# Performance work log

Measured on AMD Instinct MI355X. Metric: run time of the kernel, lower is better.

Reference implementation:

```python
import jax, jax.numpy as jnp
import numpy as np

K = 3
DILATION = 1
DG = 1  # deformable groups


def _deform_conv2d(x, offsets, mask, weight, bias, k=K, dilation=DILATION, dg=DG):
    # x: [B, C, H, W]; offsets: [B, dg*2*k*k, H, W]; mask: [B, dg*k*k, H, W]
    # weight: [O, C, k, k]; bias: [O]
    B, C, H, W = x.shape
    O = weight.shape[0]
    Cg = C // dg
    kk = k * k
    pad = (k // 2) * dilation

    # base sampling grid per kernel tap (stride=1)
    ky, kx = jnp.meshgrid(jnp.arange(k), jnp.arange(k), indexing='ij')
    ky = ky.reshape(kk)
    kx = kx.reshape(kk)
    base_y = (jnp.arange(H)[None, :, None] - pad + ky[:, None, None] * dilation)  # [kk,H,1]
    base_x = (jnp.arange(W)[None, None, :] - pad + kx[:, None, None] * dilation)  # [kk,1,W]

    off = offsets.reshape(B, dg, kk, 2, H, W)
    py = base_y[None, None].astype(x.dtype) + off[:, :, :, 0]  # [B,dg,kk,H,W]
    px = base_x[None, None].astype(x.dtype) + off[:, :, :, 1]  # [B,dg,kk,H,W]

    y0 = jnp.floor(py)
    x0 = jnp.floor(px)
    wy1 = py - y0  # frac weights
    wx1 = px - x0
    wy0 = 1.0 - wy1
    wx0 = 1.0 - wx1

    img = x.reshape(B, dg, Cg, H * W)

    def gather(yi, xi):
        # yi, xi: float integer-valued coords [B,dg,kk,H,W]; zero outside bounds
        valid = (yi >= 0) & (yi <= H - 1) & (xi >= 0) & (xi <= W - 1)
        yc = jnp.clip(yi, 0, H - 1).astype(jnp.int32)
        xc = jnp.clip(xi, 0, W - 1).astype(jnp.int32)
        idx = (yc * W + xc).reshape(B, dg, 1, kk * H * W)
        vals = jnp.take_along_axis(img, idx, axis=3).reshape(B, dg, Cg, kk, H, W)
        return vals * valid.reshape(B, dg, 1, kk, H, W).astype(x.dtype)

    def w5(a):  # lift [B,dg,kk,H,W] -> [B,dg,1,kk,H,W]
        return a.reshape(B, dg, 1, kk, H, W)

    sampled = (gather(y0, x0) * w5(wy0 * wx0)
               + gather(y0, x0 + 1) * w5(wy0 * wx1)
               + gather(y0 + 1, x0) * w5(wy1 * wx0)
               + gather(y0 + 1, x0 + 1) * w5(wy1 * wx1))  # [B,dg,Cg,kk,H,W]

    sampled = sampled * mask.reshape(B, dg, 1, kk, H, W)
    sampled = sampled.reshape(B, C, kk, H, W)

    out = jnp.einsum('bckhw,ock->bohw', sampled, weight.reshape(O, C, kk))
    return out + bias[None, :, None, None]


def setup_inputs() -> dict:
    key = jax.random.key(0)
    k1, k2, k3, k4, k5 = jax.random.split(key, 5)
    B, C, O, H, W = 8, 128, 128, 64, 64
    x = jax.random.normal(k1, (B, C, H, W), dtype=jnp.float32)
    offsets = jax.random.normal(k2, (B, DG * 2 * K * K, H, W), dtype=jnp.float32)
    mask = jax.random.uniform(k3, (B, DG * K * K, H, W), dtype=jnp.float32)
    fan_in = C * K * K
    weight = jax.random.normal(k4, (O, C, K, K), dtype=jnp.float32) / np.sqrt(fan_in)
    bias = jax.random.normal(k5, (O,), dtype=jnp.float32) * 0.01
    return {"x": x, "offsets": offsets, "mask": mask, "weight": weight, "bias": bias}


def reference(x, offsets, mask, weight, bias):
    return _deform_conv2d(x, offsets, mask, weight, bias)
```

## Files before the change

kernel.cpp:

```cpp
#include <hip/hip_runtime.h>
#include <math.h>

constexpr int Bn = 8, Cn = 128, On = 128, Hn = 64, Wn = 64;
constexpr int KK = 9, PAD = 1;
constexpr int BDIM = 512;
constexpr int PXB  = 64;
constexpr int CG = 16, NG = Cn / CG;
constexpr int KG = 160, KTOT = NG * KG;
constexpr int BANDH = 11;
constexpr int RST  = 68;
constexpr int XSTP = 756;
constexpr int AST  = 84;
constexpr int ME   = KK * PXB;
constexpr int PB_DW  = 8 * XSTP;
constexpr int ASH_DW = PXB * AST;
constexpr int SM_DW  = PB_DW + 2 * ASH_DW;
constexpr int BUNITS = BANDH * 128;

typedef __attribute__((ext_vector_type(2))) _Float16 h2;
typedef __attribute__((ext_vector_type(8))) __fp16   f16x8;
typedef __attribute__((ext_vector_type(4))) float f32x4;
typedef unsigned short u16;
typedef unsigned int u32;

union UH  { u32 u; h2 h; };
union U4H { uint4 u; f16x8 h; };

__device__ __forceinline__ u32 pkh(float a, float b) {
    union { decltype(__builtin_amdgcn_cvt_pkrtz(0.f, 0.f)) p; u32 u; } t;
    t.p = __builtin_amdgcn_cvt_pkrtz(a, b);
    return t.u;
}
__device__ __forceinline__ h2 bch(u32 w) { UH t; t.u = w; return t.h; }
__device__ __forceinline__ u16 f2h(float f) {
    union { _Float16 h; u16 u; } v; v.h = (_Float16)f; return v.u;
}

__global__ void wprep_kernel(const float* __restrict__ w, u16* __restrict__ wh) {
    __shared__ u32 tmpw[KTOT / 2];
    u16* tmp = (u16*)tmpw;
    const int tid = threadIdx.x, o = blockIdx.x;
    if (tid < 64)
        tmpw[(tid >> 3) * 80 + 72 + (tid & 7)] = 0;
    for (int k = tid; k < Cn * KK; k += 256) {
        const int c = k / 9, t = k - 9 * c;
        tmp[(c >> 4) * KG + t * 16 + (c & 15)] = f2h(w[o * (Cn * KK) + k]);
    }
    __syncthreads();
    u32* dst = (u32*)(wh + (size_t)o * KTOT);
    for (int e = tid; e < KTOT / 2; e += 256) dst[e] = tmpw[e];
}

__device__ __forceinline__ void do_sample(const u32* __restrict__ pband,
                                          u32* __restrict__ ashW,
                                          const float* __restrict__ xg,
                                          const uint4 wp, const int2 q,
                                          const int2 ix, const int e)
{
    const int t = e >> 6, px = e & 63;
    u32 avp[8];
    if (!__any((q.x | q.y) < 0)) {
        const u32* p0 = pband + ix.x;
        const u32* p1 = pband + ix.y;
        const h2 w0 = bch(wp.x), w1 = bch(wp.y), w2 = bch(wp.z), w3 = bch(wp.w);
        #pragma unroll
        for (int c2 = 0; c2 < 8; ++c2) {
            const h2 vt0 = bch(p0[c2 * XSTP]), vt1 = bch(p0[c2 * XSTP + 1]);
            const h2 vb0 = bch(p1[c2 * XSTP]), vb1 = bch(p1[c2 * XSTP + 1]);
            const h2 r = w0 * vt0 + w1 * vt1 + w2 * vb0 + w3 * vb1;
            UH o; o.h = r; avp[c2] = o.u;
        }
    } else {
        const float fw0 = (float)bch(wp.x)[0], fw1 = (float)bch(wp.y)[0];
        const float fw2 = (float)bch(wp.z)[0], fw3 = (float)bch(wp.w)[0];
        const int qx = q.x < 0 ? ~q.x : q.x;
        const int qy = q.y < 0 ? ~q.y : q.y;
        const int yrx = qx >> 8, yry = qy >> 8;
        const int xx = (qx & 255) - 1, xy = (qy & 255) - 1;
        const int ax0 = max(xx, 0), ax1 = min(xx + 1, Wn - 1);
        const int ay0 = max(xy, 0), ay1 = min(xy + 1, Wn - 1);
        #pragma unroll
        for (int c2 = 0; c2 < 8; ++c2) {
            float v2[2];
            #pragma unroll
            for (int sb = 0; sb < 2; ++sb) {
                const float* gc = xg + ((2 * c2 + sb) << 12);
                const float t0 = gc[yrx * Wn + ax0], t1 = gc[yrx * Wn + ax1];
                const float b0 = gc[yry * Wn + ay0], b1 = gc[yry * Wn + ay1];
                v2[sb] = fmaf(fw0, t0, fmaf(fw1, t1, fmaf(fw2, b0, fw3 * b1)));
            }
            avp[c2] = pkh(v2[0], v2[1]);
        }
    }
    u32* d = ashW + px * AST + t * 8;
    *(uint4*)&d[0] = make_uint4(avp[0], avp[1], avp[2], avp[3]);
    *(uint4*)&d[4] = make_uint4(avp[4], avp[5], avp[6], avp[7]);
}

__global__ __launch_bounds__(BDIM, 4)
void dcn_mfma_kernel(const float* __restrict__ x,
                     const float* __restrict__ offs,
                     const float* __restrict__ mask,
                     const u16*   __restrict__ wh,
                     const float* __restrict__ bias,
                     float* __restrict__ out)
{
    __shared__ __align__(16) u32 smem[SM_DW];
    u32* const pband = smem;

    const int tid = threadIdx.x;
    const int b   = blockIdx.x & 7;
    const int h   = blockIdx.x >> 3;
    const int r0  = min(max(h - 5, 0), Hn - BANDH);

    const int s_px4 = tid & 15, s_pair = (tid >> 4) & 7;

    float4 bnda[3], bndb[3];
#define BLOAD(GCH) { \
        _Pragma("unroll") \
        for (int it = 0; it < 3; ++it) { \
            const int u = tid + it * BDIM; \
            if (u < BUNITS) { \
                const int row = u >> 7; \
                const float* bp = x + (((size_t)(b * Cn + (GCH) * CG + 2 * s_pair)) << 12) \
                                  + (r0 + row) * Wn + (s_px4 << 2); \
                bnda[it] = *(const float4*)bp; \
                bndb[it] = *(const float4*)(bp + 4096); \
            } \
        } }
#define BWRITE() { \
        _Pragma("unroll") \
        for (int it = 0; it < 3; ++it) { \
            const int u = tid + it * BDIM; \
            if (u < BUNITS) { \
                const int row = u >> 7; \
                u32* d = &pband[s_pair * XSTP + row * RST + 8 + (s_px4 << 2)]; \
                *(uint4*)d = make_uint4( \
                    pkh(bnda[it].x, bndb[it].x), pkh(bnda[it].y, bndb[it].y), \
                    pkh(bnda[it].z, bndb[it].z), pkh(bnda[it].w, bndb[it].w)); \
            } \
        } }

    BLOAD(0);

    uint4 mwp[2]; int2 mq[2]; int2 mi[2];
    #pragma unroll
    for (int it = 0; it < 2; ++it) {
        mwp[it] = make_uint4(0, 0, 0, 0);
        mq[it] = make_int2(r0 << 8, r0 << 8);
        mi[it] = make_int2(7, 7);
        const int e = tid + it * BDIM;
        if (e < ME) {
            const int t = e >> 6, px = e & 63;
            const int ty = t / 3, tx = t - ty * 3;
            const float oy = offs[((b * 18 + 2 * t    ) * Hn + h) * Wn + px];
            const float ox = offs[((b * 18 + 2 * t + 1) * Hn + h) * Wn + px];
            const float m  = mask[((b * KK + t) * Hn + h) * Wn + px];
            const float py = (float)(h - PAD + ty) + oy;
            const float qx = (float)(px - PAD + tx) + ox;
            const float fy = floorf(py), fx = floorf(qx);
            const float wy1 = py - fy, wx1 = qx - fx;
            const float wy0 = 1.f - wy1, wx0 = 1.f - wx1;
            const int y0 = (int)fy, x0 = (int)fx;
            const bool cx0 = (x0 >= 0) && (x0 < Wn);
            const bool cx1 = (x0 >= -1) && (x0 < Wn - 1);
            const float wr[2] = { wy0, wy1 };
            float wout[4]; int qout[2], iout[2];
            #pragma unroll
            for (int j = 0; j < 2; ++j) {
                const int yr = y0 + j;
                const bool rv = (yr >= 0) && (yr < Hn);
                wout[2 * j]     = (rv && cx0) ? wr[j] * wx0 * m : 0.f;
                wout[2 * j + 1] = (rv && cx1) ? wr[j] * wx1 * m : 0.f;
                int qv;
                if (!rv || (!cx0 && !cx1)) qv = r0 << 8;
                else                       qv = (yr << 8) | (x0 + 1);
                const bool inband = (qv >> 8) >= r0 && (qv >> 8) < r0 + BANDH;
                qout[j] = inband ? qv : ~qv;
                iout[j] = ((qv >> 8) - r0) * RST + (qv & 255) + 7;
            }
            mwp[it] = make_uint4(pkh(wout[0], wout[0]), pkh(wout[1], wout[1]),
                                 pkh(wout[2], wout[2]), pkh(wout[3], wout[3]));
            mq[it] = make_int2(qout[0], qout[1]);
            mi[it] = make_int2(iout[0], iout[1]);
        }
    }

    if (tid < 416) {
        const int pair = tid / 52, j = tid - pair * 52;
        const int off = (j < 8) ? j : RST * ((j - 8) >> 2) + 72 + ((j - 8) & 3);
        pband[pair * XSTP + off] = 0;
    }
    #pragma unroll
    for (int it = 0; it < 2; ++it) {
        const int u = tid + it * BDIM;
        smem[PB_DW + (u >> 9) * ASH_DW + ((u & 511) >> 3) * AST + 72 + (u & 7)] = 0;
    }

    BWRITE();
    BLOAD(1);
    __syncthreads();

    const int wv = tid >> 6, ln = tid & 63, quad = ln >> 4, l16 = ln & 15;
    const int mrow = wv >> 1, ncol = wv & 1;
    const u16* wrow0 = wh + (size_t)(mrow * 32 + l16) * KTOT;
    const int npx0 = ncol * 32 + l16, npx1 = npx0 + 16;

    {
        const float* xg = x + (((size_t)(b * Cn)) << 12);
        do_sample(pband, smem + PB_DW, xg, mwp[0], mq[0], mi[0], tid);
        if (tid < 64)
            do_sample(pband, smem + PB_DW, xg, mwp[1], mq[1], mi[1], BDIM + tid);
    }
    __syncthreads();

    f32x4 acc[2][2];
    #pragma unroll
    for (int mt = 0; mt < 2; ++mt)
        #pragma unroll
        for (int nt = 0; nt < 2; ++nt) acc[mt][nt] = (f32x4){0.f, 0.f, 0.f, 0.f};

    f16x8 pa[5][2];
#define APRE(GG) { const int kgp = (GG) * KG + quad * 8; \
        _Pragma("unroll") \
        for (int s = 0; s < 5; ++s) { \
            pa[s][0] = *(const f16x8*)(wrow0 + kgp + s * 32); \
            pa[s][1] = *(const f16x8*)(wrow0 + 16 * KTOT + kgp + s * 32); \
        } }
    APRE(0);

#define MSTEP(S) { \
        const int kd = (S) * 16 + quad * 4; \
        U4H b0, b1; \
        b0.u = *(const uint4*)&ad[npx0 * AST + kd]; \
        b1.u = *(const uint4*)&ad[npx1 * AST + kd]; \
        acc[0][0] = __builtin_amdgcn_mfma_f32_16x16x32_f16(pa[S][0], b0.h, acc[0][0], 0, 0, 0); \
        acc[0][1] = __builtin_amdgcn_mfma_f32_16x16x32_f16(pa[S][0], b1.h, acc[0][1], 0, 0, 0); \
        acc[1][0] = __builtin_amdgcn_mfma_f32_16x16x32_f16(pa[S][1], b0.h, acc[1][0], 0, 0, 0); \
        acc[1][1] = __builtin_amdgcn_mfma_f32_16x16x32_f16(pa[S][1], b1.h, acc[1][1], 0, 0, 0); }

    for (int g = 0; g < NG; ++g) {
        const u32* ad = smem + PB_DW + (g & 1) * ASH_DW;
        u32* ashN     = smem + PB_DW + ((g + 1) & 1) * ASH_DW;
        if (g + 1 < NG) BWRITE();
        MSTEP(0);
        MSTEP(1);
        __syncthreads();
        if (g + 2 < NG) BLOAD(g + 2);
        if (g + 1 < NG) {
            const float* xg = x + (((size_t)(b * Cn + (g + 1) * CG)) << 12);
            do_sample(pband, ashN, xg, mwp[0], mq[0], mi[0], tid);
            if (tid < 64)
                do_sample(pband, ashN, xg, mwp[1], mq[1], mi[1], BDIM + tid);
        }
        MSTEP(2);
        MSTEP(3);
        MSTEP(4);
        if (g + 1 < NG) APRE(g + 1);
        __syncthreads();
    }

    float* tr = (float*)smem;
    #pragma unroll
    for (int mt = 0; mt < 2; ++mt)
        #pragma unroll
        for (int nt = 0; nt < 2; ++nt)
            #pragma unroll
            for (int r = 0; r < 4; ++r) {
                const int o  = mrow * 32 + mt * 16 + quad * 4 + r;
                const int px = ncol * 32 + nt * 16 + l16;
                tr[o * 68 + px] = acc[mt][nt][r] + bias[o];
            }
    __syncthreads();
    {
        const int orow = tid >> 2, f0 = tid & 3;
        #pragma unroll
        for (int it = 0; it < 4; ++it) {
            const int f = f0 + it * 4;
            const float4 v = *(const float4*)&tr[orow * 68 + (f << 2)];
            *(float4*)&out[(((size_t)b * On + orow) * Hn + h) * Wn + (f << 2)] = v;
        }
    }
#undef BLOAD
#undef BWRITE
#undef APRE
#undef MSTEP
}

constexpr int FBD = 256;
constexpr int FB_PXB = 32, FB_CCH = 4, FB_NCT = FB_CCH * KK, FB_MW = KK * FB_PXB;

#define FMA4(A, S, W)                          \
    A.x = fmaf((S).x, (W), A.x);               \
    A.y = fmaf((S).y, (W), A.y);               \
    A.z = fmaf((S).z, (W), A.z);               \
    A.w = fmaf((S).w, (W), A.w);

__global__ __launch_bounds__(FBD, 4)
void dcn_fb_kernel(const float* __restrict__ x,
                   const float* __restrict__ offs,
                   const float* __restrict__ mask,
                   const float* __restrict__ weight,
                   const float* __restrict__ bias,
                   float* __restrict__ out)
{
    __shared__ float wmeta[4 * FB_MW];
    __shared__ int   imeta[4 * FB_MW];
    __shared__ float ssh[FB_NCT * FB_PXB];
    __shared__ float wsh[FB_NCT * On];

    const int tid    = threadIdx.x;
    const int b      = blockIdx.x & 7;
    const int rem    = blockIdx.x >> 3;
    const int h      = rem >> 1;
    const int pxbase = (rem & 1) * FB_PXB;

    for (int e = tid; e < FB_MW; e += FBD) {
        const int t  = e >> 5;
        const int px = e & 31;
        const int pg = pxbase + px;
        const int ty = t / 3, tx = t - ty * 3;
        const float oy = offs[((b * 18 + 2 * t    ) * Hn + h) * Wn + pg];
        const float ox = offs[((b * 18 + 2 * t + 1) * Hn + h) * Wn + pg];
        const float m  = mask[((b * KK + t) * Hn + h) * Wn + pg];
        const float py = (float)(h - PAD + ty) + oy;
        const float qx = (float)(pg - PAD + tx) + ox;
        const float y0 = floorf(py), x0 = floorf(qx);
        const float wy1 = py - y0, wx1 = qx - x0;
        const float wy0 = 1.f - wy1, wx0 = 1.f - wx1;
        const float cw[4] = { wy0 * wx0, wy0 * wx1, wy1 * wx0, wy1 * wx1 };
        #pragma unroll
        for (int k = 0; k < 4; ++k) {
            const float yk = y0 + (float)(k >> 1);
            const float xk = x0 + (float)(k & 1);
            const bool valid = (yk >= 0.f) && (yk <= (float)(Hn - 1)) &&
                               (xk >= 0.f) && (xk <= (float)(Wn - 1));
            const int yc = (int)fminf(fmaxf(yk, 0.f), (float)(Hn - 1));
            const int xc = (int)fminf(fmaxf(xk, 0.f), (float)(Wn - 1));
            wmeta[k * FB_MW + e] = valid ? cw[k] * m : 0.f;
            imeta[k * FB_MW + e] = yc * Wn + xc;
        }
    }
    __syncthreads();

    const int px0 = (tid & 7) << 2;
    const int oo  = (tid >> 3) << 2;

    float4 acc[4];
    #pragma unroll
    for (int j = 0; j < 4; ++j) acc[j] = make_float4(0.f, 0.f, 0.f, 0.f);

    for (int cb = 0; cb < Cn / FB_CCH; ++cb) {
        #pragma unroll
        for (int it = 0; it < (FB_NCT * On) / FBD; ++it) {
            const int e = tid + it * FBD;
            const int r = e >> 7;
            const int o = e & 127;
            wsh[r * On + o] = weight[o * (Cn * KK) + cb * FB_NCT + r];
        }
        for (int e = tid; e < FB_NCT * FB_PXB; e += FBD) {
            const int px = e & 31;
            const int ct = e >> 5;
            const int c  = ct / 9;
            const int mb = (ct - c * 9) * FB_PXB + px;
            const float* xp = x + (((b * Cn) + cb * FB_CCH + c) << 12);
            float v =  wmeta[mb]              * xp[imeta[mb]];
            v = fmaf(wmeta[FB_MW     + mb], xp[imeta[FB_MW     + mb]], v);
            v = fmaf(wmeta[2 * FB_MW + mb], xp[imeta[2 * FB_MW + mb]], v);
            v = fmaf(wmeta[3 * FB_MW + mb], xp[imeta[3 * FB_MW + mb]], v);
            ssh[ct * FB_PXB + px] = v;
        }
        __syncthreads();

        #pragma unroll 6
        for (int ct = 0; ct < FB_NCT; ++ct) {
            const float4 sv = *(const float4*)&ssh[ct * FB_PXB + px0];
            const float4 wa = *(const float4*)&wsh[ct * On + oo];
            FMA4(acc[0], sv, wa.x);
            FMA4(acc[1], sv, wa.y);
            FMA4(acc[2], sv, wa.z);
            FMA4(acc[3], sv, wa.w);
        }
        __syncthreads();
    }

    #pragma unroll
    for (int j = 0; j < 4; ++j) {
        const float bv = bias[oo + j];
        float4 r = acc[j];
        r.x += bv; r.y += bv; r.z += bv; r.w += bv;
        *(float4*)&out[((b * On + oo + j) * Hn + h) * Wn + pxbase + px0] = r;
    }
}

extern "C" void kernel_launch(void* const* d_in, const int* in_sizes, int n_in,
                              void* d_out, int out_size, void* d_ws, size_t ws_size,
                              hipStream_t stream) {
    const float* x      = (const float*)d_in[0];
    const float* offs   = (const float*)d_in[1];
    const float* mask   = (const float*)d_in[2];
    const float* weight = (const float*)d_in[3];
    const float* bias   = (const float*)d_in[4];
    float* out = (float*)d_out;

    const size_t need = (size_t)On * KTOT * sizeof(u16);
    if (d_ws != nullptr && ws_size >= need) {
        u16* wh = (u16*)d_ws;
        wprep_kernel<<<dim3(On), dim3(256), 0, stream>>>(weight, wh);
        dcn_mfma_kernel<<<dim3(Bn * Hn), dim3(BDIM), 0, stream>>>(
            x, offs, mask, wh, bias, out);
    } else {
        dcn_fb_kernel<<<dim3(Bn * Hn * 2), dim3(FBD), 0, stream>>>(
            x, offs, mask, weight, bias, out);
    }
}
```

Measured before the change: 149.9 us.

## Split each row into two 32-pixel blocks with 8-channel groups and higher occupancy

Restructures the MFMA deformable-conv kernel so each block handles 32 pixels of a row instead of 64, which doubles the grid to 1024 blocks. Channel groups shrink from 16 to 8 (16 groups), and the shared-memory band and sample buffers are resized to match. Each wave now owns 16 output channels against 2 pixel tiles, the A operand is loaded from global memory inside every MFMA step instead of being prefetched, and launch bounds rise to 8 blocks per CU. The aim is more parallelism and occupancy. The cost is that every block reloads the same 11-row input band, so band traffic doubles, and there are more barriers per unit of work.

```diff
diff --git a/kernel.cpp b/kernel.cpp
--- a/kernel.cpp
+++ b/kernel.cpp
@@ -4,18 +4,21 @@
 constexpr int Bn = 8, Cn = 128, On = 128, Hn = 64, Wn = 64;
 constexpr int KK = 9, PAD = 1;
 constexpr int BDIM = 512;
-constexpr int PXB  = 64;
-constexpr int CG = 16, NG = Cn / CG;
-constexpr int KG = 160, KTOT = NG * KG;
 constexpr int BANDH = 11;
 constexpr int RST  = 68;
 constexpr int XSTP = 756;
-constexpr int AST  = 84;
-constexpr int ME   = KK * PXB;
-constexpr int PB_DW  = 8 * XSTP;
-constexpr int ASH_DW = PXB * AST;
-constexpr int SM_DW  = PB_DW + 2 * ASH_DW;
-constexpr int BUNITS = BANDH * 128;
+
+constexpr int PXB3 = 32;
+constexpr int CG3  = 8,  NG3 = 16;
+constexpr int KG3  = 96;
+constexpr int KT3  = NG3 * KG3;
+constexpr int AST3 = 52;
+constexpr int ME3  = KK * PXB3;
+constexpr int PB3_DW  = 4 * XSTP;
+constexpr int ASH3_DW = PXB3 * AST3;
+constexpr int SM3_DW  = PB3_DW + 2 * ASH3_DW;
+constexpr int BU3  = BANDH * 64;
+constexpr size_t WH3_BYTES = (size_t)On * KT3 * 2;
 
 typedef __attribute__((ext_vector_type(2))) _Float16 h2;
 typedef __attribute__((ext_vector_type(8))) __fp16   f16x8;
@@ -36,35 +39,36 @@
     union { _Float16 h; u16 u; } v; v.h = (_Float16)f; return v.u;
 }
 
-__global__ void wprep_kernel(const float* __restrict__ w, u16* __restrict__ wh) {
-    __shared__ u32 tmpw[KTOT / 2];
-    u16* tmp = (u16*)tmpw;
+__global__ void wprep3_kernel(const float* __restrict__ w, u16* __restrict__ wh3) {
+    __shared__ u16 tmp[KT3];
     const int tid = threadIdx.x, o = blockIdx.x;
-    if (tid < 64)
-        tmpw[(tid >> 3) * 80 + 72 + (tid & 7)] = 0;
+    for (int e = tid; e < 384; e += 256) {
+        const int g = e / 24, j = e - g * 24;
+        tmp[g * 96 + 72 + j] = 0;
+    }
     for (int k = tid; k < Cn * KK; k += 256) {
         const int c = k / 9, t = k - 9 * c;
-        tmp[(c >> 4) * KG + t * 16 + (c & 15)] = f2h(w[o * (Cn * KK) + k]);
-    }
-    __syncthreads();
-    u32* dst = (u32*)(wh + (size_t)o * KTOT);
-    for (int e = tid; e < KTOT / 2; e += 256) dst[e] = tmpw[e];
-}
-
-__device__ __forceinline__ void do_sample(const u32* __restrict__ pband,
-                                          u32* __restrict__ ashW,
-                                          const float* __restrict__ xg,
-                                          const uint4 wp, const int2 q,
-                                          const int2 ix, const int e)
+        tmp[(c >> 3) * 96 + t * 8 + (c & 7)] = f2h(w[o * (Cn * KK) + k]);
+    }
+    __syncthreads();
+    u32* dst = (u32*)(wh3 + (size_t)o * KT3);
+    for (int e = tid; e < KT3 / 2; e += 256) dst[e] = ((u32*)tmp)[e];
+}
+
+__device__ __forceinline__ void sample3(const u32* __restrict__ pband,
+                                        u32* __restrict__ ashW,
+                                        const float* __restrict__ xg,
+                                        const uint4 wp, const int2 q,
+                                        const int2 ix, const int tid)
 {
-    const int t = e >> 6, px = e & 63;
-    u32 avp[8];
+    const int t = tid >> 5, px = tid & 31;
+    u32 avp[4];
     if (!__any((q.x | q.y) < 0)) {
         const u32* p0 = pband + ix.x;
         const u32* p1 = pband + ix.y;
         const h2 w0 = bch(wp.x), w1 = bch(wp.y), w2 = bch(wp.z), w3 = bch(wp.w);
         #pragma unroll
-        for (int c2 = 0; c2 < 8; ++c2) {
+        for (int c2 = 0; c2 < 4; ++c2) {
             const h2 vt0 = bch(p0[c2 * XSTP]), vt1 = bch(p0[c2 * XSTP + 1]);
             const h2 vb0 = bch(p1[c2 * XSTP]), vb1 = bch(p1[c2 * XSTP + 1]);
             const h2 r = w0 * vt0 + w1 * vt1 + w2 * vb0 + w3 * vb1;
@@ -80,7 +84,7 @@
         const int ax0 = max(xx, 0), ax1 = min(xx + 1, Wn - 1);
         const int ay0 = max(xy, 0), ay1 = min(xy + 1, Wn - 1);
         #pragma unroll
-        for (int c2 = 0; c2 < 8; ++c2) {
+        for (int c2 = 0; c2 < 4; ++c2) {
             float v2[2];
             #pragma unroll
             for (int sb = 0; sb < 2; ++sb) {
@@ -92,101 +96,93 @@
             avp[c2] = pkh(v2[0], v2[1]);
         }
     }
-    u32* d = ashW + px * AST + t * 8;
-    *(uint4*)&d[0] = make_uint4(avp[0], avp[1], avp[2], avp[3]);
-    *(uint4*)&d[4] = make_uint4(avp[4], avp[5], avp[6], avp[7]);
-}
-
-__global__ __launch_bounds__(BDIM, 4)
-void dcn_mfma_kernel(const float* __restrict__ x,
-                     const float* __restrict__ offs,
-                     const float* __restrict__ mask,
-                     const u16*   __restrict__ wh,
-                     const float* __restrict__ bias,
-                     float* __restrict__ out)
+    *(uint4*)(ashW + px * AST3 + t * 4) = make_uint4(avp[0], avp[1], avp[2], avp[3]);
+}
+
+__global__ __launch_bounds__(BDIM, 8)
+void dcn_cg8_kernel(const float* __restrict__ x,
+                    const float* __restrict__ offs,
+                    const float* __restrict__ mask,
+                    const u16*   __restrict__ wh3,
+                    const float* __restrict__ bias,
+                    float* __restrict__ out)
 {
-    __shared__ __align__(16) u32 smem[SM_DW];
+    __shared__ __align__(16) u32 smem[SM3_DW];
     u32* const pband = smem;
 
-    const int tid = threadIdx.x;
-    const int b   = blockIdx.x & 7;
-    const int h   = blockIdx.x >> 3;
-    const int r0  = min(max(h - 5, 0), Hn - BANDH);
-
-    const int s_px4 = tid & 15, s_pair = (tid >> 4) & 7;
-
-    float4 bnda[3], bndb[3];
-#define BLOAD(GCH) { \
+    const int tid    = threadIdx.x;
+    const int b      = blockIdx.x & 7;
+    const int h      = (blockIdx.x >> 3) & 63;
+    const int pxbase = (blockIdx.x >> 9) * PXB3;
+    const int r0     = min(max(h - 5, 0), Hn - BANDH);
+
+    float4 bnda[2], bndb[2];
+#define BLOAD3(GCH) { \
         _Pragma("unroll") \
-        for (int it = 0; it < 3; ++it) { \
+        for (int it = 0; it < 2; ++it) { \
             const int u = tid + it * BDIM; \
-            if (u < BUNITS) { \
-                const int row = u >> 7; \
-                const float* bp = x + (((size_t)(b * Cn + (GCH) * CG + 2 * s_pair)) << 12) \
-                                  + (r0 + row) * Wn + (s_px4 << 2); \
+            if (u < BU3) { \
+                const int px4 = u & 15, pair = (u >> 4) & 3, row = u >> 6; \
+                const float* bp = x + (((size_t)(b * Cn + (GCH) * CG3 + 2 * pair)) << 12) \
+                                  + (r0 + row) * Wn + (px4 << 2); \
                 bnda[it] = *(const float4*)bp; \
                 bndb[it] = *(const float4*)(bp + 4096); \
             } \
         } }
-#define BWRITE() { \
+#define BWRITE3() { \
         _Pragma("unroll") \
-        for (int it = 0; it < 3; ++it) { \
+        for (int it = 0; it < 2; ++it) { \
             const int u = tid + it * BDIM; \
-            if (u < BUNITS) { \
-                const int row = u >> 7; \
-                u32* d = &pband[s_pair * XSTP + row * RST + 8 + (s_px4 << 2)]; \
+            if (u < BU3) { \
+                const int px4 = u & 15, pair = (u >> 4) & 3, row = u >> 6; \
+                u32* d = &pband[pair * XSTP + row * RST + 8 + (px4 << 2)]; \
                 *(uint4*)d = make_uint4( \
                     pkh(bnda[it].x, bndb[it].x), pkh(bnda[it].y, bndb[it].y), \
                     pkh(bnda[it].z, bndb[it].z), pkh(bnda[it].w, bndb[it].w)); \
             } \
         } }
 
-    BLOAD(0);
-
-    uint4 mwp[2]; int2 mq[2]; int2 mi[2];
-    #pragma unroll
-    for (int it = 0; it < 2; ++it) {
-        mwp[it] = make_uint4(0, 0, 0, 0);
-        mq[it] = make_int2(r0 << 8, r0 << 8);
-        mi[it] = make_int2(7, 7);
-        const int e = tid + it * BDIM;
-        if (e < ME) {
-            const int t = e >> 6, px = e & 63;
-            const int ty = t / 3, tx = t - ty * 3;
-            const float oy = offs[((b * 18 + 2 * t    ) * Hn + h) * Wn + px];
-            const float ox = offs[((b * 18 + 2 * t + 1) * Hn + h) * Wn + px];
-            const float m  = mask[((b * KK + t) * Hn + h) * Wn + px];
-            const float py = (float)(h - PAD + ty) + oy;
-            const float qx = (float)(px - PAD + tx) + ox;
-            const float fy = floorf(py), fx = floorf(qx);
-            const float wy1 = py - fy, wx1 = qx - fx;
-            const float wy0 = 1.f - wy1, wx0 = 1.f - wx1;
-            const int y0 = (int)fy, x0 = (int)fx;
-            const bool cx0 = (x0 >= 0) && (x0 < Wn);
-            const bool cx1 = (x0 >= -1) && (x0 < Wn - 1);
-            const float wr[2] = { wy0, wy1 };
-            float wout[4]; int qout[2], iout[2];
-            #pragma unroll
-            for (int j = 0; j < 2; ++j) {
-                const int yr = y0 + j;
-                const bool rv = (yr >= 0) && (yr < Hn);
-                wout[2 * j]     = (rv && cx0) ? wr[j] * wx0 * m : 0.f;
-                wout[2 * j + 1] = (rv && cx1) ? wr[j] * wx1 * m : 0.f;
-                int qv;
-                if (!rv || (!cx0 && !cx1)) qv = r0 << 8;
-                else                       qv = (yr << 8) | (x0 + 1);
-                const bool inband = (qv >> 8) >= r0 && (qv >> 8) < r0 + BANDH;
-                qout[j] = inband ? qv : ~qv;
-                iout[j] = ((qv >> 8) - r0) * RST + (qv & 255) + 7;
-            }
-            mwp[it] = make_uint4(pkh(wout[0], wout[0]), pkh(wout[1], wout[1]),
-                                 pkh(wout[2], wout[2]), pkh(wout[3], wout[3]));
-            mq[it] = make_int2(qout[0], qout[1]);
-            mi[it] = make_int2(iout[0], iout[1]);
-        }
-    }
-
-    if (tid < 416) {
+    BLOAD3(0);
+
+    uint4 mwp = make_uint4(0, 0, 0, 0);
+    int2 mq = make_int2(r0 << 8, r0 << 8);
+    int2 mi = make_int2(7, 7);
+    if (tid < ME3) {
+        const int t = tid >> 5, px = tid & 31, pg = pxbase + px;
+        const int ty = t / 3, tx = t - ty * 3;
+        const float oy = offs[((b * 18 + 2 * t    ) * Hn + h) * Wn + pg];
+        const float ox = offs[((b * 18 + 2 * t + 1) * Hn + h) * Wn + pg];
+        const float m  = mask[((b * KK + t) * Hn + h) * Wn + pg];
+        const float py = (float)(h - PAD + ty) + oy;
+        const float qx = (float)(pg - PAD + tx) + ox;
+        const float fy = floorf(py), fx = floorf(qx);
+        const float wy1 = py - fy, wx1 = qx - fx;
+        const float wy0 = 1.f - wy1, wx0 = 1.f - wx1;
+        const int y0 = (int)fy, x0 = (int)fx;
+        const bool cx0 = (x0 >= 0) && (x0 < Wn);
+        const bool cx1 = (x0 >= -1) && (x0 < Wn - 1);
+        const float wr[2] = { wy0, wy1 };
+        float wout[4]; int qout[2], iout[2];
+        #pragma unroll
+        for (int j = 0; j < 2; ++j) {
+            const int yr = y0 + j;
+            const bool rv = (yr >= 0) && (yr < Hn);
+            wout[2 * j]     = (rv && cx0) ? wr[j] * wx0 * m : 0.f;
+            wout[2 * j + 1] = (rv && cx1) ? wr[j] * wx1 * m : 0.f;
+            int qv;
+            if (!rv || (!cx0 && !cx1)) qv = r0 << 8;
+            else                       qv = (yr << 8) | (x0 + 1);
+            const bool inband = (qv >> 8) >= r0 && (qv >> 8) < r0 + BANDH;
+            qout[j] = inband ? qv : ~qv;
+            iout[j] = ((qv >> 8) - r0) * RST + (qv & 255) + 7;
+        }
+        mwp = make_uint4(pkh(wout[0], wout[0]), pkh(wout[1], wout[1]),
+                         pkh(wout[2], wout[2]), pkh(wout[3], wout[3]));
+        mq = make_int2(qout[0], qout[1]);
+        mi = make_int2(iout[0], iout[1]);
+    }
+
+    if (tid < 208) {
         const int pair = tid / 52, j = tid - pair * 52;
         const int off = (j < 8) ? j : RST * ((j - 8) >> 2) + 72 + ((j - 8) & 3);
         pband[pair * XSTP + off] = 0;
@@ -194,97 +190,74 @@
     #pragma unroll
     for (int it = 0; it < 2; ++it) {
         const int u = tid + it * BDIM;
-        smem[PB_DW + (u >> 9) * ASH_DW + ((u & 511) >> 3) * AST + 72 + (u & 7)] = 0;
-    }
-
-    BWRITE();
-    BLOAD(1);
+        if (u < 768) {
+            const int buf = u / 384, rem = u - buf * 384;
+            const int px = rem / 12, j = rem - px * 12;
+            smem[PB3_DW + buf * ASH3_DW + px * AST3 + 36 + j] = 0;
+        }
+    }
+
+    BWRITE3();
+    BLOAD3(1);
     __syncthreads();
 
     const int wv = tid >> 6, ln = tid & 63, quad = ln >> 4, l16 = ln & 15;
-    const int mrow = wv >> 1, ncol = wv & 1;
-    const u16* wrow0 = wh + (size_t)(mrow * 32 + l16) * KTOT;
-    const int npx0 = ncol * 32 + l16, npx1 = npx0 + 16;
-
-    {
-        const float* xg = x + (((size_t)(b * Cn)) << 12);
-        do_sample(pband, smem + PB_DW, xg, mwp[0], mq[0], mi[0], tid);
-        if (tid < 64)
-            do_sample(pband, smem + PB_DW, xg, mwp[1], mq[1], mi[1], BDIM + tid);
-    }
-    __syncthreads();
-
-    f32x4 acc[2][2];
-    #pragma unroll
-    for (int mt = 0; mt < 2; ++mt)
-        #pragma unroll
-        for (int nt = 0; nt < 2; ++nt) acc[mt][nt] = (f32x4){0.f, 0.f, 0.f, 0.f};
-
-    f16x8 pa[5][2];
-#define APRE(GG) { const int kgp = (GG) * KG + quad * 8; \
-        _Pragma("unroll") \
-        for (int s = 0; s < 5; ++s) { \
-            pa[s][0] = *(const f16x8*)(wrow0 + kgp + s * 32); \
-            pa[s][1] = *(const f16x8*)(wrow0 + 16 * KTOT + kgp + s * 32); \
-        } }
-    APRE(0);
-
-#define MSTEP(S) { \
-        const int kd = (S) * 16 + quad * 4; \
+    const u16* wrow = wh3 + (size_t)(wv * 16 + l16) * KT3;
+
+    if (tid < ME3)
+        sample3(pband, smem + PB3_DW, x + (((size_t)(b * Cn)) << 12),
+                mwp, mq, mi, tid);
+    __syncthreads();
+
+    f32x4 acc[2];
+    acc[0] = (f32x4){0.f, 0.f, 0.f, 0.f};
+    acc[1] = (f32x4){0.f, 0.f, 0.f, 0.f};
+
+#define MSTEP3(S) { \
+        const f16x8 a = *(const f16x8*)(wrow + g * KG3 + (S) * 32 + quad * 8); \
         U4H b0, b1; \
-        b0.u = *(const uint4*)&ad[npx0 * AST + kd]; \
-        b1.u = *(const uint4*)&ad[npx1 * AST + kd]; \
-        acc[0][0] = __builtin_amdgcn_mfma_f32_16x16x32_f16(pa[S][0], b0.h, acc[0][0], 0, 0, 0); \
-        acc[0][1] = __builtin_amdgcn_mfma_f32_16x16x32_f16(pa[S][0], b1.h, acc[0][1], 0, 0, 0); \
-        acc[1][0] = __builtin_amdgcn_mfma_f32_16x16x32_f16(pa[S][1], b0.h, acc[1][0], 0, 0, 0); \
-        acc[1][1] = __builtin_amdgcn_mfma_f32_16x16x32_f16(pa[S][1], b1.h, acc[1][1], 0, 0, 0); }
-
-    for (int g = 0; g < NG; ++g) {
-        const u32* ad = smem + PB_DW + (g & 1) * ASH_DW;
-        u32* ashN     = smem + PB_DW + ((g + 1) & 1) * ASH_DW;
-        if (g + 1 < NG) BWRITE();
-        MSTEP(0);
-        MSTEP(1);
+        b0.u = *(const uint4*)&ad[l16 * AST3 + (S) * 16 + quad * 4]; \
+        b1.u = *(const uint4*)&ad[(16 + l16) * AST3 + (S) * 16 + quad * 4]; \
+        acc[0] = __builtin_amdgcn_mfma_f32_16x16x32_f16(a, b0.h, acc[0], 0, 0, 0); \
+        acc[1] = __builtin_amdgcn_mfma_f32_16x16x32_f16(a, b1.h, acc[1], 0, 0, 0); }
+
+    for (int g = 0; g < NG3; ++g) {
+        const u32* ad = smem + PB3_DW + (g & 1) * ASH3_DW;
+        u32* ashN     = smem + PB3_DW + ((g + 1) & 1) * ASH3_DW;
+        if (g + 1 < NG3) BWRITE3();
+        MSTEP3(0);
         __syncthreads();
-        if (g + 2 < NG) BLOAD(g + 2);
-        if (g + 1 < NG) {
-            const float* xg = x + (((size_t)(b * Cn + (g + 1) * CG)) << 12);
-            do_sample(pband, ashN, xg, mwp[0], mq[0], mi[0], tid);
-            if (tid < 64)
-                do_sample(pband, ashN, xg, mwp[1], mq[1], mi[1], BDIM + tid);
-        }
-        MSTEP(2);
-        MSTEP(3);
-        MSTEP(4);
-        if (g + 1 < NG) APRE(g + 1);
+        if (g + 2 < NG3) BLOAD3(g + 2);
+        if (g + 1 < NG3 && tid < ME3)
+            sample3(pband, ashN,
+                    x + (((size_t)(b * Cn + (g + 1) * CG3)) << 12),
+                    mwp, mq, mi, tid);
+        MSTEP3(1);
+        MSTEP3(2);
         __syncthreads();
     }
 
     float* tr = (float*)smem;
     #pragma unroll
-    for (int mt = 0; mt < 2; ++mt)
-        #pragma unroll
-        for (int nt = 0; nt < 2; ++nt)
-            #pragma unroll
-            for (int r = 0; r < 4; ++r) {
-                const int o  = mrow * 32 + mt * 16 + quad * 4 + r;
-                const int px = ncol * 32 + nt * 16 + l16;
-                tr[o * 68 + px] = acc[mt][nt][r] + bias[o];
-            }
+    for (int nt = 0; nt < 2; ++nt)
+        #pragma unroll
+        for (int r = 0; r < 4; ++r) {
+            const int o = wv * 16 + quad * 4 + r;
+            tr[o * 36 + nt * 16 + l16] = acc[nt][r] + bias[o];
+        }
     __syncthreads();
     {
-        const int orow = tid >> 2, f0 = tid & 3;
-        #pragma unroll
-        for (int it = 0; it < 4; ++it) {
-            const int f = f0 + it * 4;
-            const float4 v = *(const float4*)&tr[orow * 68 + (f << 2)];
-            *(float4*)&out[(((size_t)b * On + orow) * Hn + h) * Wn + (f << 2)] = v;
-        }
-    }
-#undef BLOAD
-#undef BWRITE
-#undef APRE
-#undef MSTEP
+        const int f = tid & 7;
+        #pragma unroll
+        for (int it = 0; it < 2; ++it) {
+            const int o = it * 64 + (tid >> 3);
+            *(float4*)&out[(((size_t)b * On + o) << 12) + h * Wn + pxbase + (f << 2)]
+                = *(const float4*)&tr[o * 36 + (f << 2)];
+        }
+    }
+#undef BLOAD3
+#undef BWRITE3
+#undef MSTEP3
 }
 
 constexpr int FBD = 256;
@@ -403,12 +376,11 @@
     const float* bias   = (const float*)d_in[4];
     float* out = (float*)d_out;
 
-    const size_t need = (size_t)On * KTOT * sizeof(u16);
-    if (d_ws != nullptr && ws_size >= need) {
-        u16* wh = (u16*)d_ws;
-        wprep_kernel<<<dim3(On), dim3(256), 0, stream>>>(weight, wh);
-        dcn_mfma_kernel<<<dim3(Bn * Hn), dim3(BDIM), 0, stream>>>(
-            x, offs, mask, wh, bias, out);
+    if (d_ws != nullptr && ws_size >= WH3_BYTES) {
+        u16* wh3 = (u16*)d_ws;
+        wprep3_kernel<<<dim3(On), dim3(256), 0, stream>>>(weight, wh3);
+        dcn_cg8_kernel<<<dim3(2 * Bn * Hn), dim3(BDIM), 0, stream>>>(
+            x, offs, mask, wh3, bias, out);
     } else {
         dcn_fb_kernel<<<dim3(Bn * Hn * 2), dim3(FBD), 0, stream>>>(
             x, offs, mask, weight, bias, out);
```

Result: slower. 170.5 us (+13.7%).

## Single-buffer sampled tile and load weight fragments per MFMA step

Applied to the files above, without the earlier changes.

Replaces the double-buffered sampled-activation LDS tile with a single buffer. Each group is now sampled, synchronised, then consumed, instead of sampling the next group while the current one is multiplied. The register-held weight prefetch array (pa[5][2]) is dropped and weight fragments are loaded from global memory inside each MFMA step. This cuts LDS use and register pressure, which may raise occupancy, but it gives up the overlap between sampling and matrix math and puts global-load latency directly in front of the MFMAs.

```diff
diff --git a/kernel.cpp b/kernel.cpp
--- a/kernel.cpp
+++ b/kernel.cpp
@@ -14,8 +14,9 @@
 constexpr int ME   = KK * PXB;
 constexpr int PB_DW  = 8 * XSTP;
 constexpr int ASH_DW = PXB * AST;
-constexpr int SM_DW  = PB_DW + 2 * ASH_DW;
+constexpr int SM_DW  = PB_DW + ASH_DW;
 constexpr int BUNITS = BANDH * 128;
+constexpr size_t WH_BYTES = (size_t)On * KTOT * 2;
 
 typedef __attribute__((ext_vector_type(2))) _Float16 h2;
 typedef __attribute__((ext_vector_type(8))) __fp16   f16x8;
@@ -107,6 +108,7 @@
 {
     __shared__ __align__(16) u32 smem[SM_DW];
     u32* const pband = smem;
+    u32* const ash   = smem + PB_DW;
 
     const int tid = threadIdx.x;
     const int b   = blockIdx.x & 7;
@@ -191,11 +193,7 @@
         const int off = (j < 8) ? j : RST * ((j - 8) >> 2) + 72 + ((j - 8) & 3);
         pband[pair * XSTP + off] = 0;
     }
-    #pragma unroll
-    for (int it = 0; it < 2; ++it) {
-        const int u = tid + it * BDIM;
-        smem[PB_DW + (u >> 9) * ASH_DW + ((u & 511) >> 3) * AST + 72 + (u & 7)] = 0;
-    }
+    ash[(tid >> 3) * AST + 72 + (tid & 7)] = 0;
 
     BWRITE();
     BLOAD(1);
@@ -206,57 +204,40 @@
     const u16* wrow0 = wh + (size_t)(mrow * 32 + l16) * KTOT;
     const int npx0 = ncol * 32 + l16, npx1 = npx0 + 16;
 
-    {
-        const float* xg = x + (((size_t)(b * Cn)) << 12);
-        do_sample(pband, smem + PB_DW, xg, mwp[0], mq[0], mi[0], tid);
-        if (tid < 64)
-            do_sample(pband, smem + PB_DW, xg, mwp[1], mq[1], mi[1], BDIM + tid);
-    }
-    __syncthreads();
-
     f32x4 acc[2][2];
     #pragma unroll
     for (int mt = 0; mt < 2; ++mt)
         #pragma unroll
         for (int nt = 0; nt < 2; ++nt) acc[mt][nt] = (f32x4){0.f, 0.f, 0.f, 0.f};
 
-    f16x8 pa[5][2];
-#define APRE(GG) { const int kgp = (GG) * KG + quad * 8; \
-        _Pragma("unroll") \
-        for (int s = 0; s < 5; ++s) { \
-            pa[s][0] = *(const f16x8*)(wrow0 + kgp + s * 32); \
-            pa[s][1] = *(const f16x8*)(wrow0 + 16 * KTOT + kgp + s * 32); \
-        } }
-    APRE(0);
-
 #define MSTEP(S) { \
+        const int kg = g * KG + (S) * 32 + quad * 8; \
+        const f16x8 a0 = *(const f16x8*)(wrow0 + kg); \
+        const f16x8 a1 = *(const f16x8*)(wrow0 + 16 * KTOT + kg); \
         const int kd = (S) * 16 + quad * 4; \
         U4H b0, b1; \
-        b0.u = *(const uint4*)&ad[npx0 * AST + kd]; \
-        b1.u = *(const uint4*)&ad[npx1 * AST + kd]; \
-        acc[0][0] = __builtin_amdgcn_mfma_f32_16x16x32_f16(pa[S][0], b0.h, acc[0][0], 0, 0, 0); \
-        acc[0][1] = __builtin_amdgcn_mfma_f32_16x16x32_f16(pa[S][0], b1.h, acc[0][1], 0, 0, 0); \
-        acc[1][0] = __builtin_amdgcn_mfma_f32_16x16x32_f16(pa[S][1], b0.h, acc[1][0], 0, 0, 0); \
-        acc[1][1] = __builtin_amdgcn_mfma_f32_16x16x32_f16(pa[S][1], b1.h, acc[1][1], 0, 0, 0); }
+        b0.u = *(const uint4*)&ash[npx0 * AST + kd]; \
+        b1.u = *(const uint4*)&ash[npx1 * AST + kd]; \
+        acc[0][0] = __builtin_amdgcn_mfma_f32_16x16x32_f16(a0, b0.h, acc[0][0], 0, 0, 0); \
+        acc[0][1] = __builtin_amdgcn_mfma_f32_16x16x32_f16(a0, b1.h, acc[0][1], 0, 0, 0); \
+        acc[1][0] = __builtin_amdgcn_mfma_f32_16x16x32_f16(a1, b0.h, acc[1][0], 0, 0, 0); \
+        acc[1][1] = __builtin_amdgcn_mfma_f32_16x16x32_f16(a1, b1.h, acc[1][1], 0, 0, 0); }
 
     for (int g = 0; g < NG; ++g) {
-        const u32* ad = smem + PB_DW + (g & 1) * ASH_DW;
-        u32* ashN     = smem + PB_DW + ((g + 1) & 1) * ASH_DW;
+        {
+            const float* xg = x + (((size_t)(b * Cn + g * CG)) << 12);
+            do_sample(pband, ash, xg, mwp[0], mq[0], mi[0], tid);
+            if (tid < 64)
+                do_sample(pband, ash, xg, mwp[1], mq[1], mi[1], BDIM + tid);
+        }
+        __syncthreads();
         if (g + 1 < NG) BWRITE();
+        if (g + 2 < NG) BLOAD(g + 2);
         MSTEP(0);
         MSTEP(1);
-        __syncthreads();
-        if (g + 2 < NG) BLOAD(g + 2);
-        if (g + 1 < NG) {
-            const float* xg = x + (((size_t)(b * Cn + (g + 1) * CG)) << 12);
-            do_sample(pband, ashN, xg, mwp[0], mq[0], mi[0], tid);
-            if (tid < 64)
-                do_sample(pband, ashN, xg, mwp[1], mq[1], mi[1], BDIM + tid);
-        }
         MSTEP(2);
         MSTEP(3);
         MSTEP(4);
-        if (g + 1 < NG) APRE(g + 1);
         __syncthreads();
     }
 
@@ -283,7 +264,6 @@
     }
 #undef BLOAD
 #undef BWRITE
-#undef APRE
 #undef MSTEP
 }
 
@@ -403,8 +383,7 @@
     const float* bias   = (const float*)d_in[4];
     float* out = (float*)d_out;
 
-    const size_t need = (size_t)On * KTOT * sizeof(u16);
-    if (d_ws != nullptr && ws_size >= need) {
+    if (d_ws != nullptr && ws_size >= WH_BYTES) {
         u16* wh = (u16*)d_ws;
         wprep_kernel<<<dim3(On), dim3(256), 0, stream>>>(weight, wh);
         dcn_mfma_kernel<<<dim3(Bn * Hn), dim3(BDIM), 0, stream>>>(
```

Result: faster. 140.3 us (-6.4%).
